# Optimization experiments

Hardware: AMD Instinct MI355X
Metric: run time of the kernel (lower is better)

Reference implementation:

```python
import jax, jax.numpy as jnp
import numpy as np

S, HID, H, KV, D = 2048, 3584, 16, 8, 256
WINDOW = 1024
SOFTCAP = 50.0
SCALING = 256 ** (-0.5)  # query_pre_attn_scalar ** -0.5
EPS = 1e-6
ROPE_THETA = 10000.0


def _rope_tables(seq_len, dim, theta):
    inv_freq = 1.0 / (theta ** (np.arange(0, dim, 2, dtype=np.float32) / dim))
    t = np.arange(seq_len, dtype=np.float32)
    freqs = np.outer(t, inv_freq)            # [S, D/2]
    emb = np.concatenate([freqs, freqs], -1)  # [S, D]
    return jnp.asarray(np.cos(emb)), jnp.asarray(np.sin(emb))


def setup_inputs() -> dict:
    key = jax.random.key(0)
    ks = jax.random.split(key, 3)
    hidden_states = jax.random.normal(ks[0], (S, HID), jnp.float32)
    w_qkv = jax.random.normal(ks[1], (HID, (H + 2 * KV) * D), jnp.float32) * (HID ** -0.5)
    w_o = jax.random.normal(ks[2], (H * D, HID), jnp.float32) * ((H * D) ** -0.5)
    q_norm_w = jnp.zeros((D,), jnp.float32)  # gemma norm stores weight as (1 + w)
    k_norm_w = jnp.zeros((D,), jnp.float32)
    cos, sin = _rope_tables(S, D, ROPE_THETA)
    return {"hidden_states": hidden_states, "w_qkv": w_qkv, "w_o": w_o,
            "q_norm_w": q_norm_w, "k_norm_w": k_norm_w, "cos": cos, "sin": sin}


def _rms_norm(x, w):
    # gemma-style: fp32 norm, scale by (1 + w); x: [S, h, D]
    xf = x.astype(jnp.float32)
    var = jnp.mean(xf * xf, axis=-1, keepdims=True)
    return (xf * jax.lax.rsqrt(var + EPS) * (1.0 + w)).astype(x.dtype)


def _rotate_half(x):
    x1, x2 = jnp.split(x, 2, axis=-1)
    return jnp.concatenate([-x2, x1], axis=-1)


def _apply_rope(x, cos, sin):
    # x: [S, h, D]; cos/sin: [S, D]
    c = cos[:, None, :]
    s = sin[:, None, :]
    return x * c + _rotate_half(x) * s


def reference(hidden_states, w_qkv, w_o, q_norm_w, k_norm_w, cos, sin):
    qkv = hidden_states @ w_qkv                      # [S, (H+2KV)*D]
    q = qkv[:, : H * D].reshape(S, H, D)
    k = qkv[:, H * D: (H + KV) * D].reshape(S, KV, D)
    v = qkv[:, (H + KV) * D:].reshape(S, KV, D)

    q = _rms_norm(q, q_norm_w)                       # gemma3 q_norm
    k = _rms_norm(k, k_norm_w)                       # gemma3 k_norm
    q = _apply_rope(q, cos, sin)
    k = _apply_rope(k, cos, sin)

    # GQA: expand KV heads to H
    rep = H // KV
    k = jnp.repeat(k, rep, axis=1)                   # [S, H, D]
    v = jnp.repeat(v, rep, axis=1)

    scores = jnp.einsum('shd,thd->hst', q, k) * SCALING  # [H, S, S]
    scores = SOFTCAP * jnp.tanh(scores / SOFTCAP)        # logit softcapping

    i = jnp.arange(S)[:, None]
    j = jnp.arange(S)[None, :]
    allowed = (j <= i) & ((i - j) < WINDOW)              # causal + sliding window
    scores = jnp.where(allowed[None], scores, jnp.float32(-1e30))

    attn = jax.nn.softmax(scores, axis=-1)
    out = jnp.einsum('hst,thd->shd', attn, v).reshape(S, H * D)
    return out @ w_o                                     # [S, HID]
```

## Files before the change

kernel.cpp:

```cpp
#include <hip/hip_runtime.h>
#include <hip/hip_bf16.h>
#include <math.h>

typedef __attribute__((ext_vector_type(8))) short short8;
typedef __attribute__((ext_vector_type(4))) float floatx4;
typedef unsigned short u16;

typedef __attribute__((address_space(1))) const void* gas_ptr;
typedef __attribute__((address_space(3))) void* las_ptr;

__device__ __forceinline__ float bf2f(u16 h) {
  union { unsigned u; float f; } v; v.u = ((unsigned)h) << 16; return v.f;
}
__device__ __forceinline__ u16 f2bf(float f) {
  union { float f; unsigned u; } v; v.f = f;
  unsigned r = v.u + 0x7FFFu + ((v.u >> 16) & 1u);
  return (u16)(r >> 16);
}
__device__ __forceinline__ float ldf_dyn(const void* p, size_t i, bool f32) {
  return f32 ? ((const float*)p)[i] : bf2f(((const u16*)p)[i]);
}
__device__ __forceinline__ short8 load8_dyn(const void* p, size_t idx, bool f32) {
  if (f32) {
    const float* f = (const float*)p;
    float4 a = *(const float4*)(f + idx);
    float4 b = *(const float4*)(f + idx + 4);
    short8 r;
    r[0] = (short)f2bf(a.x); r[1] = (short)f2bf(a.y);
    r[2] = (short)f2bf(a.z); r[3] = (short)f2bf(a.w);
    r[4] = (short)f2bf(b.x); r[5] = (short)f2bf(b.y);
    r[6] = (short)f2bf(b.z); r[7] = (short)f2bf(b.w);
    return r;
  }
  return *(const short8*)((const u16*)p + idx);
}
__device__ __forceinline__ void gl_lds16(const u16* g, u16* l) {
  __builtin_amdgcn_global_load_lds((gas_ptr)g, (las_ptr)l, 16, 0, 0);
}

__global__ void probe_dtype_kernel(const void* hidden, int* flag) {
  __shared__ int cnt;
  if (threadIdx.x == 0) cnt = 0;
  __syncthreads();
  const u16* h = (const u16*)hidden;
  int local = 0;
  for (int i = threadIdx.x; i < 8192; i += 256) {
    u16 u = h[i];
    int e = (u >> 7) & 0xFF;
    if ((e >= 64 && e <= 160) || (u & 0x7FFF) == 0) local++;
  }
  atomicAdd(&cnt, local);
  __syncthreads();
  if (threadIdx.x == 0) *flag = (cnt < 7700) ? 1 : 0;
}

__global__ __launch_bounds__(256) void convert_dyn_kernel(
    const void* __restrict__ src, u16* __restrict__ dst, size_t n,
    const int* __restrict__ flagp)
{
  const bool f32 = (*flagp != 0);
  size_t i = ((size_t)blockIdx.x * 256 + threadIdx.x) * 8;
  if (i < n) *(short8*)(dst + i) = load8_dyn(src, i, f32);
}

__global__ __launch_bounds__(256) void transpose_dyn_kernel(
    const void* __restrict__ src, u16* __restrict__ dst, int R, int C,
    const int* __restrict__ flagp)
{
  const bool f32 = (*flagp != 0);
  const int c0 = blockIdx.x * 64, r0 = blockIdx.y * 64;
  __shared__ __attribute__((aligned(16))) u16 T[64][72];
  const int tid = threadIdx.x;
#pragma unroll
  for (int i = 0; i < 2; i++) {
    int t = tid + i * 256;
    int r = t >> 3, cc = (t & 7) << 3;
    *(short8*)(&T[r][cc]) = load8_dyn(src, (size_t)(r0 + r) * C + c0 + cc, f32);
  }
  __syncthreads();
#pragma unroll
  for (int i = 0; i < 2; i++) {
    int t = tid + i * 256;
    int cr = t >> 3, rc = (t & 7) << 3;
    __attribute__((aligned(16))) u16 tmp[8];
#pragma unroll
    for (int j = 0; j < 8; j++) tmp[j] = T[rc + j][cr];
    *(short8*)(dst + (size_t)(c0 + cr) * R + r0 + rc) = *(const short8*)tmp;
  }
}

#define BAR() __builtin_amdgcn_s_barrier()
#define SCB() __builtin_amdgcn_sched_barrier(0)
#define LGKM0() do { asm volatile("s_waitcnt lgkmcnt(0)" ::: "memory"); SCB(); } while (0)
#define LGKMC(n) do { asm volatile("s_waitcnt lgkmcnt(" #n ")" ::: "memory"); SCB(); } while (0)
#define VMW(n) do { asm volatile("s_waitcnt vmcnt(" #n ")" ::: "memory"); SCB(); } while (0)

#define STG_AU(s, u, t) \
  gl_lds16(pa + (size_t)((u) * 64) * K + (size_t)(t) * 64, \
           ldsw + (s) * 32768 + (u) * 4096)
#define STG_BU(s, u, t) \
  gl_lds16(pb + (size_t)((u) * 64) * K + (size_t)(t) * 64, \
           ldsw + (s) * 32768 + 16384 + (u) * 4096)

#define RD_FA(A, s, miH) do { \
  _Pragma("unroll") \
  for (int m2 = 0; m2 < 4; m2++) { \
    const u16* _r = LDS + (s) * 32768 + wm * 8192 + (miH) * 4096 + m2 * 1024 + lane15 * 64; \
    A[m2][0] = *(const short8*)(_r + colA0); \
    A[m2][1] = *(const short8*)(_r + colA1); \
  } \
} while (0)
#define RD_FB(s, niH) do { \
  _Pragma("unroll") \
  for (int n2 = 0; n2 < 2; n2++) { \
    const u16* _r = LDS + (s) * 32768 + 16384 + wn * 4096 + (niH) * 2048 + n2 * 1024 + lane15 * 64; \
    fb[niH][n2][0] = *(const short8*)(_r + colA0); \
    fb[niH][n2][1] = *(const short8*)(_r + colA1); \
  } \
} while (0)
#define MFMA_Q(A, miH, niH) do { \
  __builtin_amdgcn_s_setprio(1); \
  _Pragma("unroll") \
  for (int m2 = 0; m2 < 4; m2++) \
    _Pragma("unroll") \
    for (int n2 = 0; n2 < 2; n2++) { \
      acc[(miH) * 4 + m2][(niH) * 2 + n2] = __builtin_amdgcn_mfma_f32_16x16x32_bf16( \
          A[m2][0], fb[niH][n2][0], acc[(miH) * 4 + m2][(niH) * 2 + n2], 0, 0, 0); \
      acc[(miH) * 4 + m2][(niH) * 2 + n2] = __builtin_amdgcn_mfma_f32_16x16x32_bf16( \
          A[m2][1], fb[niH][n2][1], acc[(miH) * 4 + m2][(niH) * 2 + n2], 0, 0, 0); \
    } \
  __builtin_amdgcn_s_setprio(0); \
  SCB(); \
} while (0)

__global__ __launch_bounds__(512, 2) void gemm8p_kernel(
    const u16* __restrict__ A, const u16* __restrict__ BT, u16* __restrict__ C,
    int M, int N, int K)
{
  __shared__ __attribute__((aligned(16))) u16 LDS[65536];
  const int tid = threadIdx.x;
  const int wave = tid >> 6, lane = tid & 63;
  const int lane15 = lane & 15, quad = lane >> 4;
  const int wm = wave >> 2, wn = wave & 3;
  const int m0 = blockIdx.y * 256, n0 = blockIdx.x * 256;

  const int rloc = wave * 8 + (lane >> 3);
  const int sxor = lane >> 3;
  const int csw = ((lane & 7) ^ sxor) * 8;
  const u16* pa = A + (size_t)(m0 + rloc) * K + csw;
  const u16* pb = BT + (size_t)(n0 + rloc) * K + csw;
  u16* ldsw = LDS + wave * 512;

  const int swz = lane15 & 7;
  const int colA0 = (quad ^ swz) * 8;
  const int colA1 = ((4 + quad) ^ swz) * 8;

  floatx4 acc[8][4];
#pragma unroll
  for (int i = 0; i < 8; i++)
#pragma unroll
    for (int j = 0; j < 4; j++) acc[i][j] = (floatx4){0.f, 0.f, 0.f, 0.f};
  short8 fa0[4][2], fa1[4][2], fb[2][2][2];

  const int NT = K >> 6, NI = NT >> 1;

  STG_AU(0, 0, 0); STG_AU(0, 2, 0);
  STG_BU(0, 0, 0); STG_BU(0, 1, 0);
  STG_BU(0, 2, 0); STG_BU(0, 3, 0);
  STG_AU(0, 1, 0); STG_AU(0, 3, 0);
  STG_AU(1, 0, 1); STG_AU(1, 2, 1);
  STG_BU(1, 0, 1); STG_BU(1, 1, 1);
  STG_BU(1, 2, 1); STG_BU(1, 3, 1);
  VMW(8);
  BAR();

  for (int i = 0; i < NI - 1; i++) {
    const int t1 = 2 * i + 1, t2 = 2 * i + 2, t3 = 2 * i + 3;
    RD_FA(fa0, 0, 0); RD_FB(0, 0);
    SCB();
    STG_AU(1, 1, t1); STG_AU(1, 3, t1);
    RD_FB(0, 1);
    BAR(); LGKMC(4); MFMA_Q(fa0, 0, 0); VMW(8); BAR();
    RD_FA(fa1, 0, 1);
    SCB();
    STG_AU(0, 0, t2); STG_AU(0, 2, t2);
    BAR(); LGKMC(8); MFMA_Q(fa0, 0, 1); BAR();
    STG_BU(0, 0, t2); STG_BU(0, 1, t2);
    BAR(); LGKM0(); MFMA_Q(fa1, 1, 1); BAR();
    STG_BU(0, 2, t2); STG_BU(0, 3, t2);
    BAR(); MFMA_Q(fa1, 1, 0); VMW(8); BAR();
    RD_FA(fa0, 1, 0); RD_FB(1, 0);
    SCB();
    STG_AU(0, 1, t2); STG_AU(0, 3, t2);
    RD_FB(1, 1);
    BAR(); LGKMC(4); MFMA_Q(fa0, 0, 0); VMW(8); BAR();
    RD_FA(fa1, 1, 1);
    SCB();
    STG_AU(1, 0, t3); STG_AU(1, 2, t3);
    BAR(); LGKMC(8); MFMA_Q(fa0, 0, 1); BAR();
    STG_BU(1, 0, t3); STG_BU(1, 1, t3);
    BAR(); LGKM0(); MFMA_Q(fa1, 1, 1); BAR();
    STG_BU(1, 2, t3); STG_BU(1, 3, t3);
    BAR(); MFMA_Q(fa1, 1, 0); VMW(8); BAR();
  }

  {
    const int tL = NT - 1;
    RD_FA(fa0, 0, 0); RD_FB(0, 0);
    STG_AU(1, 1, tL); STG_AU(1, 3, tL);
    BAR(); LGKM0(); MFMA_Q(fa0, 0, 0); BAR();
    RD_FB(0, 1);
    BAR(); LGKM0(); MFMA_Q(fa0, 0, 1); VMW(8); BAR();
    RD_FA(fa1, 0, 1);
    BAR(); LGKM0(); MFMA_Q(fa1, 1, 1); BAR();
    BAR(); MFMA_Q(fa1, 1, 0); VMW(2); BAR();
    RD_FA(fa0, 1, 0); RD_FB(1, 0);
    BAR(); LGKM0(); MFMA_Q(fa0, 0, 0); BAR();
    RD_FB(1, 1);
    BAR(); LGKM0(); MFMA_Q(fa0, 0, 1); VMW(0); BAR();
    RD_FA(fa1, 1, 1);
    BAR(); LGKM0(); MFMA_Q(fa1, 1, 1); BAR();
    BAR(); MFMA_Q(fa1, 1, 0);
  }

#pragma unroll
  for (int mi = 0; mi < 8; mi++)
#pragma unroll
    for (int rr = 0; rr < 4; rr++) {
      int m = m0 + wm * 128 + mi * 16 + quad * 4 + rr;
      u16* crow = C + (size_t)m * N + n0 + wn * 64;
#pragma unroll
      for (int ni = 0; ni < 4; ni++) crow[ni * 16 + lane15] = f2bf(acc[mi][ni][rr]);
    }
}

#define NSTG_A(s, u, t) \
  gl_lds16(pa + (size_t)((u) * 64) * K + (size_t)(t) * 64, \
           ldsw + (s) * 24576 + (u) * 4096)
#define NSTG_B(s, u, t) \
  gl_lds16(pb + (size_t)((u) * 64) * K + (size_t)(t) * 64, \
           ldsw + (s) * 24576 + 8192 + (u) * 4096)

#define NRD_FA(A, s, miH) do { \
  _Pragma("unroll") \
  for (int m2 = 0; m2 < 2; m2++) { \
    const u16* _r = LDS + (s) * 24576 + wm * 4096 + (miH) * 2048 + m2 * 1024 + lane15 * 64; \
    A[m2][0] = *(const short8*)(_r + colA0); \
    A[m2][1] = *(const short8*)(_r + colA1); \
  } \
} while (0)
#define NRD_FB(s, niH) do { \
  _Pragma("unroll") \
  for (int n2 = 0; n2 < 2; n2++) { \
    const u16* _r = LDS + (s) * 24576 + 8192 + wn * 4096 + (niH) * 2048 + n2 * 1024 + lane15 * 64; \
    fb[niH][n2][0] = *(const short8*)(_r + colA0); \
    fb[niH][n2][1] = *(const short8*)(_r + colA1); \
  } \
} while (0)
#define NMFMA_Q(A, miH, niH) do { \
  __builtin_amdgcn_s_setprio(1); \
  _Pragma("unroll") \
  for (int m2 = 0; m2 < 2; m2++) \
    _Pragma("unroll") \
    for (int n2 = 0; n2 < 2; n2++) { \
      acc[(miH) * 2 + m2][(niH) * 2 + n2] = __builtin_amdgcn_mfma_f32_16x16x32_bf16( \
          A[m2][0], fb[niH][n2][0], acc[(miH) * 2 + m2][(niH) * 2 + n2], 0, 0, 0); \
      acc[(miH) * 2 + m2][(niH) * 2 + n2] = __builtin_amdgcn_mfma_f32_16x16x32_bf16( \
          A[m2][1], fb[niH][n2][1], acc[(miH) * 2 + m2][(niH) * 2 + n2], 0, 0, 0); \
    } \
  __builtin_amdgcn_s_setprio(0); \
  SCB(); \
} while (0)

__global__ __launch_bounds__(512, 2) void gemm8pn_kernel(
    const u16* __restrict__ A, const u16* __restrict__ BT, void* __restrict__ C,
    int M, int N, int K, const int* __restrict__ flagp, int cdyn)
{
  __shared__ __attribute__((aligned(16))) u16 LDS[49152];
  const int tid = threadIdx.x;
  const int wave = tid >> 6, lane = tid & 63;
  const int lane15 = lane & 15, quad = lane >> 4;
  const int wm = wave >> 2, wn = wave & 3;
  const int m0 = blockIdx.y * 128, n0 = blockIdx.x * 256;

  const int rloc = wave * 8 + (lane >> 3);
  const int sxor = lane >> 3;
  const int csw = ((lane & 7) ^ sxor) * 8;
  const u16* pa = A + (size_t)(m0 + rloc) * K + csw;
  const u16* pb = BT + (size_t)(n0 + rloc) * K + csw;
  u16* ldsw = LDS + wave * 512;

  const int swz = lane15 & 7;
  const int colA0 = (quad ^ swz) * 8;
  const int colA1 = ((4 + quad) ^ swz) * 8;

  floatx4 acc[4][4];
#pragma unroll
  for (int i = 0; i < 4; i++)
#pragma unroll
    for (int j = 0; j < 4; j++) acc[i][j] = (floatx4){0.f, 0.f, 0.f, 0.f};
  short8 fa0[2][2], fa1[2][2], fb[2][2][2];

  const int NT = K >> 6, NI = NT >> 1;

  NSTG_B(0, 0, 0); NSTG_B(0, 1, 0); NSTG_B(0, 2, 0); NSTG_B(0, 3, 0);
  NSTG_A(0, 0, 0); NSTG_A(0, 1, 0);
  NSTG_B(1, 0, 1); NSTG_B(1, 1, 1); NSTG_B(1, 2, 1); NSTG_B(1, 3, 1);
  NSTG_A(1, 0, 1); NSTG_A(1, 1, 1);
  VMW(6);
  BAR();

  for (int i = 0; i < NI - 1; i++) {
    const int t2 = 2 * i + 2, t3 = 2 * i + 3;
    NRD_FA(fa0, 0, 0); NRD_FB(0, 0);
    SCB();
    NRD_FB(0, 1);
    BAR(); LGKMC(4); NMFMA_Q(fa0, 0, 0); BAR();
    NRD_FA(fa1, 0, 1);
    BAR(); LGKMC(4); NMFMA_Q(fa0, 0, 1); BAR();
    NSTG_B(0, 0, t2); NSTG_B(0, 1, t2);
    BAR(); LGKM0(); NMFMA_Q(fa1, 1, 1); BAR();
    NSTG_B(0, 2, t2); NSTG_B(0, 3, t2); NSTG_A(0, 0, t2); NSTG_A(0, 1, t2);
    BAR(); NMFMA_Q(fa1, 1, 0); VMW(6); BAR();
    NRD_FA(fa0, 1, 0); NRD_FB(1, 0);
    SCB();
    NRD_FB(1, 1);
    BAR(); LGKMC(4); NMFMA_Q(fa0, 0, 0); BAR();
    NRD_FA(fa1, 1, 1);
    BAR(); LGKMC(4); NMFMA_Q(fa0, 0, 1); BAR();
    NSTG_B(1, 0, t3); NSTG_B(1, 1, t3);
    BAR(); LGKM0(); NMFMA_Q(fa1, 1, 1); BAR();
    NSTG_B(1, 2, t3); NSTG_B(1, 3, t3); NSTG_A(1, 0, t3); NSTG_A(1, 1, t3);
    BAR(); NMFMA_Q(fa1, 1, 0); VMW(6); BAR();
  }

  {
    NRD_FA(fa0, 0, 0); NRD_FB(0, 0);
    BAR(); LGKM0(); NMFMA_Q(fa0, 0, 0); BAR();
    NRD_FB(0, 1);
    BAR(); LGKM0(); NMFMA_Q(fa0, 0, 1); BAR();
    NRD_FA(fa1, 0, 1);
    BAR(); LGKM0(); NMFMA_Q(fa1, 1, 1); BAR();
    BAR(); NMFMA_Q(fa1, 1, 0); VMW(0); BAR();
    NRD_FA(fa0, 1, 0); NRD_FB(1, 0);
    BAR(); LGKM0(); NMFMA_Q(fa0, 0, 0); BAR();
    NRD_FB(1, 1);
    BAR(); LGKM0(); NMFMA_Q(fa0, 0, 1); BAR();
    NRD_FA(fa1, 1, 1);
    BAR(); LGKM0(); NMFMA_Q(fa1, 1, 1); BAR();
    NMFMA_Q(fa1, 1, 0);
  }

  const bool cf32 = cdyn && (*flagp != 0);
  if (cf32) {
    float* Cf = (float*)C;
#pragma unroll
    for (int mi = 0; mi < 4; mi++)
#pragma unroll
      for (int rr = 0; rr < 4; rr++) {
        int m = m0 + wm * 64 + mi * 16 + quad * 4 + rr;
        float* crow = Cf + (size_t)m * N + n0 + wn * 64;
#pragma unroll
        for (int ni = 0; ni < 4; ni++) crow[ni * 16 + lane15] = acc[mi][ni][rr];
      }
  } else {
    u16* Cb = (u16*)C;
#pragma unroll
    for (int mi = 0; mi < 4; mi++)
#pragma unroll
      for (int rr = 0; rr < 4; rr++) {
        int m = m0 + wm * 64 + mi * 16 + quad * 4 + rr;
        u16* crow = Cb + (size_t)m * N + n0 + wn * 64;
#pragma unroll
        for (int ni = 0; ni < 4; ni++) crow[ni * 16 + lane15] = f2bf(acc[mi][ni][rr]);
      }
  }
}

__global__ __launch_bounds__(256) void normrope_kernel(
    u16* __restrict__ qkv, const void* __restrict__ qw,
    const void* __restrict__ kw, const void* __restrict__ cosb,
    const void* __restrict__ sinb, const int* __restrict__ flagp)
{
  const bool f32 = (*flagp != 0);
  const int s = blockIdx.x;
  const int wave = threadIdx.x >> 6, lane = threadIdx.x & 63;
  const int hh = blockIdx.y * 4 + wave;
  const int col = (hh < 16) ? hh * 256 : 4096 + (hh - 16) * 256;
  const void* w = (hh < 16) ? qw : kw;
  u16* row = qkv + (size_t)s * 8192 + col;

  float x[4];
#pragma unroll
  for (int j = 0; j < 4; j++) x[j] = bf2f(row[lane + j * 64]);

  float ss = x[0] * x[0] + x[1] * x[1] + x[2] * x[2] + x[3] * x[3];
#pragma unroll
  for (int off = 32; off > 0; off >>= 1) ss += __shfl_xor(ss, off);
  float inv = rsqrtf(ss * (1.0f / 256.0f) + 1e-6f);

  float y[4];
#pragma unroll
  for (int j = 0; j < 4; j++)
    y[j] = x[j] * inv * (1.0f + ldf_dyn(w, lane + j * 64, f32));
  float rot[4] = {-y[2], -y[3], y[0], y[1]};
#pragma unroll
  for (int j = 0; j < 4; j++) {
    int d = lane + j * 64;
    float c = ldf_dyn(cosb, (size_t)s * 256 + d, f32);
    float sn = ldf_dyn(sinb, (size_t)s * 256 + d, f32);
    row[d] = f2bf(y[j] * c + rot[j] * sn);
  }
}

__global__ __launch_bounds__(256) void vtrans_kernel(
    const u16* __restrict__ qkv, u16* __restrict__ vT)
{
  const int s0 = blockIdx.x * 64, d0 = blockIdx.y * 64, kv = blockIdx.z;
  __shared__ __attribute__((aligned(16))) u16 T[64][72];
  const int tid = threadIdx.x;
#pragma unroll
  for (int i = 0; i < 2; i++) {
    int c = tid + i * 256;
    int r = c >> 3, dc = (c & 7) << 3;
    *(short8*)(&T[r][dc]) =
        *(const short8*)(qkv + (size_t)(s0 + r) * 8192 + 6144 + kv * 256 + d0 + dc);
  }
  __syncthreads();
#pragma unroll
  for (int i = 0; i < 2; i++) {
    int c = tid + i * 256;
    int dr = c >> 3, sc = (c & 7) << 3;
    __attribute__((aligned(16))) u16 tmp[8];
#pragma unroll
    for (int j = 0; j < 8; j++) tmp[j] = T[sc + j][dr];
    *(short8*)(vT + (size_t)kv * 524288 + (size_t)(d0 + dr) * 2048 + s0 + sc) =
        *(const short8*)tmp;
  }
}

__global__ __launch_bounds__(256) void attn_kernel(
    const u16* __restrict__ qkv, const u16* __restrict__ vT,
    u16* __restrict__ aout)
{
  const int h = blockIdx.y, kvh = h >> 1;
  const int q0 = blockIdx.x * 64;
  const int tid = threadIdx.x;
  const int wave = tid >> 6, lane = tid & 63;
  const int lane15 = lane & 15, quad = lane >> 4;

  __shared__ __attribute__((aligned(16))) u16 KVs[256 * 72];
  __shared__ __attribute__((aligned(16))) u16 Ps[4][16 * 72];

  short8 aq[8];
  const u16* qrow = qkv + (size_t)(q0 + wave * 16 + lane15) * 8192 + h * 256;
#pragma unroll
  for (int kt = 0; kt < 8; kt++)
    aq[kt] = *(const short8*)(qrow + kt * 32 + quad * 8);

  floatx4 zero = {0.0f, 0.0f, 0.0f, 0.0f};
  floatx4 accO[16];
#pragma unroll
  for (int i = 0; i < 16; i++) accO[i] = zero;
  float lR[4] = {0.0f, 0.0f, 0.0f, 0.0f};

  const int iRow = q0 + wave * 16 + quad * 4;
  const int kb_lo = (q0 >= 1023) ? ((q0 - 1023) >> 6) : 0;
  const int kb_hi = q0 >> 6;

  for (int kb = kb_lo; kb <= kb_hi; kb++) {
    const int t0 = kb << 6;
#pragma unroll
    for (int i = 0; i < 8; i++) {
      int c = tid + i * 256;
      int r = c >> 5, dc = (c & 31) << 3;
      *(short8*)(&KVs[r * 264 + dc]) =
          *(const short8*)(qkv + (size_t)(t0 + r) * 8192 + 4096 + kvh * 256 + dc);
    }
    __syncthreads();

    const int relHi = q0 + 16 * wave + 15 - t0;
    const int relLo = q0 + 16 * wave - 1023 - t0;
    const int niHiR = relHi >> 4;
    const int niHi = (niHiR > 3) ? 3 : niHiR;
    int niLo = relLo >> 4; if (niLo < 0) niLo = 0;
    const int ktHiR = relHi >> 5;
    const int ktHi = (ktHiR > 1) ? 1 : ktHiR;
    int ktLo = relLo >> 5; if (ktLo < 0) ktLo = 0;

    float pv[4][4];
#pragma unroll
    for (int ni = 0; ni < 4; ni++) {
      if (ni < niLo || ni > niHi) {
        pv[ni][0] = pv[ni][1] = pv[ni][2] = pv[ni][3] = 0.0f;
        continue;
      }
      floatx4 sAcc = zero;
#pragma unroll
      for (int kt = 0; kt < 8; kt++) {
        short8 bk = *(const short8*)(&KVs[(ni * 16 + lane15) * 264 + kt * 32 + quad * 8]);
        sAcc = __builtin_amdgcn_mfma_f32_16x16x32_bf16(aq[kt], bk, sAcc, 0, 0, 0);
      }
#pragma unroll
      for (int r = 0; r < 4; r++) {
        float x = sAcc[r] * 0.00125f;
        float ax = __builtin_fabsf(x);
        float e2 = __expf(ax + ax);
        float t = 1.0f - 2.0f * __builtin_amdgcn_rcpf(e2 + 1.0f);
        float sv = copysignf(t, x) * 50.0f;
        int i_ = iRow + r;
        int j_ = t0 + ni * 16 + lane15;
        bool ok = (j_ <= i_) && (i_ - j_ < 1024);
        pv[ni][r] = ok ? __expf(sv) : 0.0f;
      }
    }
#pragma unroll
    for (int r = 0; r < 4; r++)
      lR[r] += pv[0][r] + pv[1][r] + pv[2][r] + pv[3][r];

#pragma unroll
    for (int ni = 0; ni < 4; ni++)
#pragma unroll
      for (int r = 0; r < 4; r++)
        Ps[wave][(quad * 4 + r) * 72 + ni * 16 + lane15] = f2bf(pv[ni][r]);
    __syncthreads();

#pragma unroll
    for (int i = 0; i < 8; i++) {
      int c = tid + i * 256;
      int dr = c >> 3, tc = (c & 7) << 3;
      *(short8*)(&KVs[dr * 72 + tc]) =
          *(const short8*)(vT + (size_t)kvh * 524288 + (size_t)dr * 2048 + t0 + tc);
    }
    __syncthreads();

#pragma unroll
    for (int ktile = 0; ktile < 2; ktile++) {
      if (ktile < ktLo || ktile > ktHi) continue;
      short8 ap = *(const short8*)(&Ps[wave][lane15 * 72 + ktile * 32 + quad * 8]);
#pragma unroll
      for (int ni = 0; ni < 16; ni++) {
        short8 bv = *(const short8*)(&KVs[(ni * 16 + lane15) * 72 + ktile * 32 + quad * 8]);
        accO[ni] = __builtin_amdgcn_mfma_f32_16x16x32_bf16(ap, bv, accO[ni], 0, 0, 0);
      }
    }
    __syncthreads();
  }

#pragma unroll
  for (int r = 0; r < 4; r++) {
    float l = lR[r];
    l += __shfl_xor(l, 1);
    l += __shfl_xor(l, 2);
    l += __shfl_xor(l, 4);
    l += __shfl_xor(l, 8);
    float invl = 1.0f / l;
    u16* orow = aout + (size_t)(q0 + wave * 16 + quad * 4 + r) * 4096 + h * 256;
#pragma unroll
    for (int ni = 0; ni < 16; ni++)
      orow[ni * 16 + lane15] = f2bf(accO[ni][r] * invl);
  }
}

extern "C" void kernel_launch(void* const* d_in, const int* in_sizes, int n_in,
                              void* d_out, int out_size, void* d_ws, size_t ws_size,
                              hipStream_t stream)
{
  const void* hidden = d_in[0];
  const void* w_qkv  = d_in[1];
  const void* w_o    = d_in[2];
  const void* q_w    = d_in[3];
  const void* k_w    = d_in[4];
  const void* cosb   = d_in[5];
  const void* sinb   = d_in[6];

  char* ws = (char*)d_ws;
  int* flag = (int*)ws;                                   ws += 256;
  u16* qkv  = (u16*)ws;  ws += (size_t)2048 * 8192 * 2;
  u16* vT   = (u16*)ws;  ws += (size_t)8 * 256 * 2048 * 2;
  u16* aout = (u16*)ws;  ws += (size_t)2048 * 4096 * 2;
  u16* hb   = (u16*)ws;  ws += (size_t)2048 * 3584 * 2;
  u16* wT   = (u16*)ws;

  probe_dtype_kernel<<<1, 256, 0, stream>>>(hidden, flag);
  convert_dyn_kernel<<<3584, 256, 0, stream>>>(hidden, hb, (size_t)2048 * 3584, flag);
  transpose_dyn_kernel<<<dim3(128, 56), 256, 0, stream>>>(w_qkv, wT, 3584, 8192, flag);
  gemm8p_kernel<<<dim3(32, 8), 512, 0, stream>>>(hb, wT, qkv, 2048, 8192, 3584);
  normrope_kernel<<<dim3(2048, 6), 256, 0, stream>>>(qkv, q_w, k_w, cosb, sinb, flag);
  transpose_dyn_kernel<<<dim3(56, 64), 256, 0, stream>>>(w_o, wT, 4096, 3584, flag);
  vtrans_kernel<<<dim3(32, 4, 8), 256, 0, stream>>>(qkv, vT);
  attn_kernel<<<dim3(32, 16), 256, 0, stream>>>(qkv, vT, aout);
  gemm8pn_kernel<<<dim3(14, 16), 512, 0, stream>>>(aout, wT, d_out, 2048, 3584, 4096, flag, 1);
}
```

Baseline: 612.4 us.

## Skip bf16 input copy, split K/V LDS buffers, relax GEMM launch bounds

When the input is already bf16, the convert kernel now exits early and the QKV GEMM reads the raw hidden buffer directly instead of a copied one. In the attention kernel, K and V get separate shared-memory tiles so both are loaded together before one barrier, removing a second load phase and barrier per tile. Both GEMMs drop their launch-bounds occupancy hint from 2 to 1 block per CU, giving the compiler more registers at the cost of possible occupancy. Attention LDS use grows, which may reduce how many attention blocks fit per CU.

```diff
diff --git a/kernel.cpp b/kernel.cpp
--- a/kernel.cpp
+++ b/kernel.cpp
@@ -58,9 +58,9 @@
     const void* __restrict__ src, u16* __restrict__ dst, size_t n,
     const int* __restrict__ flagp)
 {
-  const bool f32 = (*flagp != 0);
+  if (*flagp == 0) return;
   size_t i = ((size_t)blockIdx.x * 256 + threadIdx.x) * 8;
-  if (i < n) *(short8*)(dst + i) = load8_dyn(src, i, f32);
+  if (i < n) *(short8*)(dst + i) = load8_dyn(src, i, true);
 }
 
 __global__ __launch_bounds__(256) void transpose_dyn_kernel(
@@ -94,6 +94,8 @@
 #define LGKM0() do { asm volatile("s_waitcnt lgkmcnt(0)" ::: "memory"); SCB(); } while (0)
 #define LGKMC(n) do { asm volatile("s_waitcnt lgkmcnt(" #n ")" ::: "memory"); SCB(); } while (0)
 #define VMW(n) do { asm volatile("s_waitcnt vmcnt(" #n ")" ::: "memory"); SCB(); } while (0)
+#define PRIO1() __builtin_amdgcn_s_setprio(1)
+#define PRIO0() do { __builtin_amdgcn_s_setprio(0); SCB(); } while (0)
 
 #define STG_AU(s, u, t) \
   gl_lds16(pa + (size_t)((u) * 64) * K + (size_t)(t) * 64, \
@@ -119,7 +121,7 @@
   } \
 } while (0)
 #define MFMA_Q(A, miH, niH) do { \
-  __builtin_amdgcn_s_setprio(1); \
+  PRIO1(); \
   _Pragma("unroll") \
   for (int m2 = 0; m2 < 4; m2++) \
     _Pragma("unroll") \
@@ -129,13 +131,13 @@
       acc[(miH) * 4 + m2][(niH) * 2 + n2] = __builtin_amdgcn_mfma_f32_16x16x32_bf16( \
           A[m2][1], fb[niH][n2][1], acc[(miH) * 4 + m2][(niH) * 2 + n2], 0, 0, 0); \
     } \
-  __builtin_amdgcn_s_setprio(0); \
-  SCB(); \
+  PRIO0(); \
 } while (0)
 
-__global__ __launch_bounds__(512, 2) void gemm8p_kernel(
-    const u16* __restrict__ A, const u16* __restrict__ BT, u16* __restrict__ C,
-    int M, int N, int K)
+__global__ __launch_bounds__(512, 1) void gemm8p_kernel(
+    const void* __restrict__ Araw, const u16* __restrict__ Ahb,
+    const u16* __restrict__ BT, u16* __restrict__ C,
+    int M, int N, int K, const int* __restrict__ flagp)
 {
   __shared__ __attribute__((aligned(16))) u16 LDS[65536];
   const int tid = threadIdx.x;
@@ -144,10 +146,12 @@
   const int wm = wave >> 2, wn = wave & 3;
   const int m0 = blockIdx.y * 256, n0 = blockIdx.x * 256;
 
+  const u16* Abase = (*flagp != 0) ? Ahb : (const u16*)Araw;
+
   const int rloc = wave * 8 + (lane >> 3);
   const int sxor = lane >> 3;
   const int csw = ((lane & 7) ^ sxor) * 8;
-  const u16* pa = A + (size_t)(m0 + rloc) * K + csw;
+  const u16* pa = Abase + (size_t)(m0 + rloc) * K + csw;
   const u16* pb = BT + (size_t)(n0 + rloc) * K + csw;
   u16* ldsw = LDS + wave * 512;
 
@@ -258,7 +262,7 @@
   } \
 } while (0)
 #define NMFMA_Q(A, miH, niH) do { \
-  __builtin_amdgcn_s_setprio(1); \
+  PRIO1(); \
   _Pragma("unroll") \
   for (int m2 = 0; m2 < 2; m2++) \
     _Pragma("unroll") \
@@ -268,11 +272,10 @@
       acc[(miH) * 2 + m2][(niH) * 2 + n2] = __builtin_amdgcn_mfma_f32_16x16x32_bf16( \
           A[m2][1], fb[niH][n2][1], acc[(miH) * 2 + m2][(niH) * 2 + n2], 0, 0, 0); \
     } \
-  __builtin_amdgcn_s_setprio(0); \
-  SCB(); \
+  PRIO0(); \
 } while (0)
 
-__global__ __launch_bounds__(512, 2) void gemm8pn_kernel(
+__global__ __launch_bounds__(512, 1) void gemm8pn_kernel(
     const u16* __restrict__ A, const u16* __restrict__ BT, void* __restrict__ C,
     int M, int N, int K, const int* __restrict__ flagp, int cdyn)
 {
@@ -449,7 +452,8 @@
   const int wave = tid >> 6, lane = tid & 63;
   const int lane15 = lane & 15, quad = lane >> 4;
 
-  __shared__ __attribute__((aligned(16))) u16 KVs[256 * 72];
+  __shared__ __attribute__((aligned(16))) u16 Ks[64 * 264];
+  __shared__ __attribute__((aligned(16))) u16 Vs[256 * 72];
   __shared__ __attribute__((aligned(16))) u16 Ps[4][16 * 72];
 
   short8 aq[8];
@@ -474,8 +478,15 @@
     for (int i = 0; i < 8; i++) {
       int c = tid + i * 256;
       int r = c >> 5, dc = (c & 31) << 3;
-      *(short8*)(&KVs[r * 264 + dc]) =
+      *(short8*)(&Ks[r * 264 + dc]) =
           *(const short8*)(qkv + (size_t)(t0 + r) * 8192 + 4096 + kvh * 256 + dc);
+    }
+#pragma unroll
+    for (int i = 0; i < 8; i++) {
+      int c = tid + i * 256;
+      int dr = c >> 3, tc = (c & 7) << 3;
+      *(short8*)(&Vs[dr * 72 + tc]) =
+          *(const short8*)(vT + (size_t)kvh * 524288 + (size_t)dr * 2048 + t0 + tc);
     }
     __syncthreads();
 
@@ -498,7 +509,7 @@
       floatx4 sAcc = zero;
 #pragma unroll
       for (int kt = 0; kt < 8; kt++) {
-        short8 bk = *(const short8*)(&KVs[(ni * 16 + lane15) * 264 + kt * 32 + quad * 8]);
+        short8 bk = *(const short8*)(&Ks[(ni * 16 + lane15) * 264 + kt * 32 + quad * 8]);
         sAcc = __builtin_amdgcn_mfma_f32_16x16x32_bf16(aq[kt], bk, sAcc, 0, 0, 0);
       }
 #pragma unroll
@@ -526,21 +537,12 @@
     __syncthreads();
 
 #pragma unroll
-    for (int i = 0; i < 8; i++) {
-      int c = tid + i * 256;
-      int dr = c >> 3, tc = (c & 7) << 3;
-      *(short8*)(&KVs[dr * 72 + tc]) =
-          *(const short8*)(vT + (size_t)kvh * 524288 + (size_t)dr * 2048 + t0 + tc);
-    }
-    __syncthreads();
-
-#pragma unroll
     for (int ktile = 0; ktile < 2; ktile++) {
       if (ktile < ktLo || ktile > ktHi) continue;
       short8 ap = *(const short8*)(&Ps[wave][lane15 * 72 + ktile * 32 + quad * 8]);
 #pragma unroll
       for (int ni = 0; ni < 16; ni++) {
-        short8 bv = *(const short8*)(&KVs[(ni * 16 + lane15) * 72 + ktile * 32 + quad * 8]);
+        short8 bv = *(const short8*)(&Vs[(ni * 16 + lane15) * 72 + ktile * 32 + quad * 8]);
         accO[ni] = __builtin_amdgcn_mfma_f32_16x16x32_bf16(ap, bv, accO[ni], 0, 0, 0);
       }
     }
@@ -585,7 +587,7 @@
   probe_dtype_kernel<<<1, 256, 0, stream>>>(hidden, flag);
   convert_dyn_kernel<<<3584, 256, 0, stream>>>(hidden, hb, (size_t)2048 * 3584, flag);
   transpose_dyn_kernel<<<dim3(128, 56), 256, 0, stream>>>(w_qkv, wT, 3584, 8192, flag);
-  gemm8p_kernel<<<dim3(32, 8), 512, 0, stream>>>(hb, wT, qkv, 2048, 8192, 3584);
+  gemm8p_kernel<<<dim3(32, 8), 512, 0, stream>>>(hidden, hb, wT, qkv, 2048, 8192, 3584, flag);
   normrope_kernel<<<dim3(2048, 6), 256, 0, stream>>>(qkv, q_w, k_w, cosb, sinb, flag);
   transpose_dyn_kernel<<<dim3(56, 64), 256, 0, stream>>>(w_o, wT, 4096, 3584, flag);
   vtrans_kernel<<<dim3(32, 4, 8), 256, 0, stream>>>(qkv, vT);
```

Measured after the change: 647.6 us. +5.7%, slower.
